# Optimization experiments

Hardware: AMD Instinct MI355X
Metric: run time of the kernel (lower is better)

The kernel has to match this reference:

```python
import jax, jax.numpy as jnp
import numpy as np

B, T, D, H = 1024, 365, 24, 128
OUT_DIMS = (1, 3, 3, 2)
GRU_IN = (D, D + 1, 2 * H, 2 * H)


def _uniform(k, shape, bound):
    return jax.random.uniform(k, shape, jnp.float32, -bound, bound)


def setup_inputs() -> dict:
    key = jax.random.key(0)
    inp = {"x": jax.random.normal(jax.random.fold_in(key, 0), (B, T, D), jnp.float32)}
    s = 1.0 / float(np.sqrt(H))  # torch GRUCell/Linear default init scale
    i = 1
    for c in range(4):
        inp[f"Wih{c+1}"] = _uniform(jax.random.fold_in(key, i), (3 * H, GRU_IN[c]), s); i += 1
        inp[f"Whh{c+1}"] = _uniform(jax.random.fold_in(key, i), (3 * H, H), s); i += 1
        inp[f"bih{c+1}"] = _uniform(jax.random.fold_in(key, i), (3 * H,), s); i += 1
        inp[f"bhh{c+1}"] = _uniform(jax.random.fold_in(key, i), (3 * H,), s); i += 1
        inp[f"Wfc{c+1}"] = _uniform(jax.random.fold_in(key, i), (OUT_DIMS[c], H), s); i += 1
        inp[f"bfc{c+1}"] = _uniform(jax.random.fold_in(key, i), (OUT_DIMS[c],), s); i += 1
    return inp


def _gru_cell(xt, h, Wih, Whh, bih, bhh):
    # PyTorch GRUCell: r,z,n gate order
    gi = xt @ Wih.T + bih
    gh = h @ Whh.T + bhh
    ir, iz, inn = jnp.split(gi, 3, axis=-1)
    hr, hz, hn = jnp.split(gh, 3, axis=-1)
    r = jax.nn.sigmoid(ir + hr)
    z = jax.nn.sigmoid(iz + hz)
    n = jnp.tanh(inn + r * hn)
    return (1.0 - z) * n + z * h


def _forward(x, Wih1, Whh1, bih1, bhh1, Wfc1, bfc1,
             Wih2, Whh2, bih2, bhh2, Wfc2, bfc2,
             Wih3, Whh3, bih3, bhh3, Wfc3, bfc3,
             Wih4, Whh4, bih4, bhh4, Wfc4, bfc4):
    b = x.shape[0]
    sg = jax.lax.stop_gradient
    h0 = jnp.zeros((b, H), x.dtype)
    lai0 = jnp.zeros((b, 1), x.dtype)  # LAI_previous starts at zero, always detached

    def step(carry, xt):
        h1, h2, h3, h4, lai = carry
        h1 = _gru_cell(xt, h1, Wih1, Whh1, bih1, bhh1)
        h2 = _gru_cell(jnp.concatenate([xt, lai], axis=1), h2, Wih2, Whh2, bih2, bhh2)
        o1 = h1 @ Wfc1.T + bfc1
        o2 = h2 @ Wfc2.T + bfc2
        h3 = _gru_cell(jnp.concatenate([sg(h1), sg(h2)], axis=1), h3, Wih3, Whh3, bih3, bhh3)
        o3 = h3 @ Wfc3.T + bfc3
        h4 = _gru_cell(jnp.concatenate([sg(h1), sg(h3)], axis=1), h4, Wih4, Whh4, bih4, bhh4)
        o4 = h4 @ Wfc4.T + bfc4
        lai = sg(o4[:, :1])
        return (h1, h2, h3, h4, lai), (jnp.concatenate([o1, o2, o3, o4], axis=1), h1, h2, h3, h4)

    (h1f, h2f, h3f, h4f, _), ys = jax.lax.scan(step, (h0, h0, h0, h0, lai0), jnp.swapaxes(x, 0, 1))
    out_t, hT1, hT2, hT3, hT4 = ys  # each [T, B, .]
    to_bt = lambda a: jnp.swapaxes(a, 0, 1)
    return (to_bt(out_t), h1f, h2f, h3f, h4f, to_bt(hT1), to_bt(hT2), to_bt(hT3), to_bt(hT4))


def reference(x, Wih1, Whh1, bih1, bhh1, Wfc1, bfc1,
              Wih2, Whh2, bih2, bhh2, Wfc2, bfc2,
              Wih3, Whh3, bih3, bhh3, Wfc3, bfc3,
              Wih4, Whh4, bih4, bhh4, Wfc4, bfc4):
    return _forward(x, Wih1, Whh1, bih1, bhh1, Wfc1, bfc1,
                    Wih2, Whh2, bih2, bhh2, Wfc2, bfc2,
                    Wih3, Whh3, bih3, bhh3, Wfc3, bfc3,
                    Wih4, Whh4, bih4, bhh4, Wfc4, bfc4)
```

## Files before the change

kernel.cpp:

```cpp
#include <hip/hip_runtime.h>
#include <hip/hip_bf16.h>

#define B_ 1024
#define T_ 365
#define D_ 24
#define H_ 128
#define NG 32
#define NS 8
#define GB 32

#define SLICE_EL 52224
#define ARENA_EL (8 * SLICE_EL)

typedef __attribute__((ext_vector_type(8))) short bf16x8;
typedef __attribute__((ext_vector_type(4))) float f32x4;

__device__ __align__(16) unsigned short g_arena[ARENA_EL];
__device__ __align__(16) unsigned g_mb[4][NG][2048];
__device__ unsigned g_flags[NG][4];
__device__ unsigned g_tick[8];

#define MFMA(a, b, c) __builtin_amdgcn_mfma_f32_16x16x32_bf16((a), (b), (c), 0, 0, 0)

__device__ __forceinline__ bf16x8 ldw(const unsigned short* p) {
  return *(const bf16x8*)p;
}
__device__ __forceinline__ unsigned short f2b(float f) {
  union { __hip_bfloat16 h; unsigned short u; } cv;
  cv.h = __float2bfloat16(f);
  return cv.u;
}
__device__ __forceinline__ float b2f(unsigned short u) {
  union { float f; unsigned int u32; } cv;
  cv.u32 = ((unsigned int)u) << 16;
  return cv.f;
}
__device__ __forceinline__ float sigmoidf_(float x) { return 1.f / (1.f + __expf(-x)); }
__device__ __forceinline__ float tanhf_(float x) {
  float e = __expf(2.f * x);
  return 1.f - 2.f / (e + 1.f);
}

__device__ __forceinline__ void st_l2(unsigned* p, unsigned v) {
  asm volatile("global_store_dword %0, %1, off sc0" :: "v"(p), "v"(v) : "memory");
}
__device__ __forceinline__ unsigned ld_dev(const unsigned* p) {
  unsigned v;
  asm volatile("global_load_dword %0, %1, off sc0 sc1\n\ts_waitcnt vmcnt(0)"
               : "=v"(v) : "v"(p) : "memory");
  return v;
}

__global__ void prep_weights(const float* wih1, const float* wih2,
                             const float* wih3, const float* wih4,
                             const float* whh1, const float* whh2,
                             const float* whh3, const float* whh4) {
  int i = blockIdx.x * blockDim.x + threadIdx.x;
  if (i < NG * 4) ((unsigned*)g_flags)[i] = 0;
  if (i < 8) g_tick[i] = 0;
  if (i >= ARENA_EL) return;
  int s = i / SLICE_EL, r = i % SLICE_EL;
  int tile = r >> 9, wi = r & 511;
  int khi = wi >> 7, nlo = (wi >> 3) & 15, e = wi & 7;
  float v = 0.f;
  if (tile < 3) {
    int row = tile * 128 + s * 16 + nlo, k = khi * 8 + e;
    if (k < 24) v = wih1[row * 24 + k];
  } else if (tile < 6) {
    int row = (tile - 3) * 128 + s * 16 + nlo, k = khi * 8 + e;
    if (k < 25) v = wih2[row * 25 + k];
  } else if (tile < 18) {
    int tt = tile - 6; int row = (tt >> 2) * 128 + s * 16 + nlo;
    v = whh1[row * 128 + (tt & 3) * 32 + khi * 8 + e];
  } else if (tile < 30) {
    int tt = tile - 18; int row = (tt >> 2) * 128 + s * 16 + nlo;
    v = whh2[row * 128 + (tt & 3) * 32 + khi * 8 + e];
  } else if (tile < 54) {
    int tt = tile - 30; int row = (tt >> 3) * 128 + s * 16 + nlo;
    v = wih3[row * 256 + (tt & 7) * 32 + khi * 8 + e];
  } else if (tile < 66) {
    int tt = tile - 54; int row = (tt >> 2) * 128 + s * 16 + nlo;
    v = whh3[row * 128 + (tt & 3) * 32 + khi * 8 + e];
  } else if (tile < 90) {
    int tt = tile - 66; int row = (tt >> 3) * 128 + s * 16 + nlo;
    v = wih4[row * 256 + (tt & 7) * 32 + khi * 8 + e];
  } else {
    int tt = tile - 90; int row = (tt >> 2) * 128 + s * 16 + nlo;
    v = whh4[row * 128 + (tt & 3) * 32 + khi * 8 + e];
  }
  g_arena[i] = f2b(v);
}

struct P {
  const float* x;
  const float* bih[4];
  const float* bhh[4];
  const float* wfc[4];
  const float* bfc[4];
  float* out;
  float* hf[4];
  float* hT[4];
};

__device__ __forceinline__ void gsync(int g, int st, unsigned target) {
  asm volatile("s_waitcnt vmcnt(0)" ::: "memory");
  __syncthreads();
  if (threadIdx.x == 0) {
    __hip_atomic_fetch_add(&g_flags[g][st], 1u, __ATOMIC_RELAXED, __HIP_MEMORY_SCOPE_AGENT);
    const unsigned* fp = &g_flags[g][st];
    unsigned v = ld_dev(fp);
    unsigned spins = 0;
    while (v < target && ++spins < (1u << 22)) {
      __builtin_amdgcn_s_sleep(2);
      v = ld_dev(fp);
    }
  }
  __syncthreads();
}

#define L_WSL  0u
#define L_HBUF 104448u
#define L_PSUM 137216u
#define L_XA   145408u
#define L_FCW  147456u
#define SMEMB  152064u

__global__ __launch_bounds__(256, 1) void gru_main(P p) {
  extern __shared__ __align__(16) unsigned char smem[];
  unsigned short* wsl = (unsigned short*)(smem + L_WSL);
  unsigned short* hbuf = (unsigned short*)(smem + L_HBUF);
  float* psum = (float*)(smem + L_PSUM);
  unsigned short* xa = (unsigned short*)(smem + L_XA);
  float (*fcw)[H_] = (float (*)[H_])(smem + L_FCW);

  const int tid = threadIdx.x;
  const int lane = tid & 63;
  const int w = tid >> 6;
  const int nlo = lane & 15, khi = lane >> 4;

  int* meta = (int*)psum;
  if (tid == 0) {
    unsigned xcc = __builtin_amdgcn_s_getreg((3 << 11) | 20) & 7;
    unsigned tk = __hip_atomic_fetch_add(&g_tick[xcc], 1u,
                                         __ATOMIC_RELAXED, __HIP_MEMORY_SCOPE_AGENT);
    tk &= 31;
    meta[0] = (int)(xcc * 4 + (tk >> 3));
    meta[1] = (int)(tk & 7);
  }
  __syncthreads();
  const int g = meta[0], s = meta[1];
  __syncthreads();

  const int b0 = g * GB;
  const int wkoff = khi * 128 + nlo * 8;
  const int hkoff = khi * 256 + nlo * 8;
  const int row = tid >> 3, cp = tid & 7;
  const int col0 = s * 16 + cp * 2;
  const int mbw = (col0 >> 3) * 128 + row * 4 + ((col0 & 7) >> 1);

  { const uint4* srcw = (const uint4*)(g_arena + s * SLICE_EL);
    uint4* dstw = (uint4*)wsl;
    for (int i = tid; i < SLICE_EL / 8; i += 256) dstw[i] = srcw[i]; }
  for (int i = tid; i < 8192; i += 256) ((unsigned*)hbuf)[i] = 0;
  for (int i = tid; i < 1024; i += 256) {
    int kg = i >> 8, rem = i & 255, r2 = rem >> 3, e = i & 7;
    int c = kg * 8 + e;
    unsigned short vv = 0;
    if (c < 24) vv = f2b(p.x[(size_t)(b0 + r2) * (T_ * D_) + c]);
    xa[i] = vv;
  }
  for (int i = tid; i < 9 * H_; i += 256) {
    int rw = i >> 7, k = i & 127;
    const float* srcf; int lr;
    if (rw == 0)      { srcf = p.wfc[0]; lr = 0; }
    else if (rw < 4)  { srcf = p.wfc[1]; lr = rw - 1; }
    else if (rw < 7)  { srcf = p.wfc[2]; lr = rw - 4; }
    else              { srcf = p.wfc[3]; lr = rw - 7; }
    fcw[rw][k] = srcf[lr * H_ + k];
  }

  float bR[4][2], bZ[4][2], bI[4][2], bHn[4][2], hreg[4][2];
#pragma unroll
  for (int c = 0; c < 4; ++c)
#pragma unroll
    for (int j = 0; j < 2; ++j) {
      int cc = col0 + j;
      bR[c][j]  = p.bih[c][cc] + p.bhh[c][cc];
      bZ[c][j]  = p.bih[c][H_ + cc] + p.bhh[c][H_ + cc];
      bI[c][j]  = p.bih[c][2 * H_ + cc];
      bHn[c][j] = p.bhh[c][2 * H_ + cc];
      hreg[c][j] = 0.f;
    }
  const float bfc7 = p.bfc[3][0];
  const float bfc8 = p.bfc[3][1];
  int fc_c = 0; float fcb = 0.f;
  if (s == 0)      { fc_c = 0; fcb = p.bfc[0][0]; }
  else if (s < 4)  { fc_c = 1; fcb = p.bfc[1][s - 1]; }
  else if (s < 7)  { fc_c = 2; fcb = p.bfc[2][s - 4]; }

  float* hTp[4];
#pragma unroll
  for (int c = 0; c < 4; ++c)
    hTp[c] = p.hT[c] + (size_t)(b0 + row) * (T_ * H_) + col0;
  float* outp = p.out + (size_t)(b0 + row) * (T_ * 9);

  const f32x4 zf = {0.f, 0.f, 0.f, 0.f};

#define WF(tt)        ldw(wsl + (tt) * 512 + wkoff)
#define HF(c, kc, mt) ldw(hbuf + (c) * 4096 + (kc) * 1024 + (mt) * 128 + hkoff)
#define XF(mt)        ldw(xa + (mt) * 128 + hkoff)
#define PWR(slot, mt, v) do { \
  float* pp_ = psum + (slot) * 512 + (mt) * 256 + khi * 64 + nlo; \
  pp_[0] = (v)[0]; pp_[16] = (v)[1]; pp_[32] = (v)[2]; pp_[48] = (v)[3]; \
} while (0)

#define STAGE_A(C, TWX, THX) do { \
  if (w < 2) { \
    _Pragma("unroll") \
    for (int mt = 0; mt < 2; ++mt) { \
      f32x4 acc = MFMA(XF(mt), WF((TWX) + w), zf); \
      _Pragma("unroll") \
      for (int kc = 0; kc < 4; ++kc) acc = MFMA(HF(C, kc, mt), WF((THX) + w * 4 + kc), acc); \
      PWR(w, mt, acc); \
    } \
  } else if (w == 2) { \
    _Pragma("unroll") \
    for (int mt = 0; mt < 2; ++mt) { f32x4 acc = MFMA(XF(mt), WF((TWX) + 2), zf); PWR(2, mt, acc); } \
  } else { \
    _Pragma("unroll") \
    for (int mt = 0; mt < 2; ++mt) { \
      f32x4 acc = zf; \
      _Pragma("unroll") \
      for (int kc = 0; kc < 4; ++kc) acc = MFMA(HF(C, kc, mt), WF((THX) + 8 + kc), acc); \
      PWR(3, mt, acc); \
    } \
  } \
} while (0)

#define STAGE_BC(CA, CB, CH, TWX, THX) do { \
  if (w < 2) { \
    _Pragma("unroll") \
    for (int mt = 0; mt < 2; ++mt) { \
      f32x4 acc = zf; \
      _Pragma("unroll") \
      for (int kc = 0; kc < 4; ++kc) acc = MFMA(HF(CA, kc, mt), WF((TWX) + w * 8 + kc), acc); \
      _Pragma("unroll") \
      for (int kc = 0; kc < 4; ++kc) acc = MFMA(HF(CB, kc, mt), WF((TWX) + w * 8 + 4 + kc), acc); \
      _Pragma("unroll") \
      for (int kc = 0; kc < 4; ++kc) acc = MFMA(HF(CH, kc, mt), WF((THX) + w * 4 + kc), acc); \
      PWR(w, mt, acc); \
    } \
  } else if (w == 2) { \
    _Pragma("unroll") \
    for (int mt = 0; mt < 2; ++mt) { \
      f32x4 acc = zf; \
      _Pragma("unroll") \
      for (int kc = 0; kc < 4; ++kc) acc = MFMA(HF(CA, kc, mt), WF((TWX) + 16 + kc), acc); \
      _Pragma("unroll") \
      for (int kc = 0; kc < 4; ++kc) acc = MFMA(HF(CB, kc, mt), WF((TWX) + 16 + 4 + kc), acc); \
      PWR(2, mt, acc); \
    } \
  } else { \
    _Pragma("unroll") \
    for (int mt = 0; mt < 2; ++mt) { \
      f32x4 acc = zf; \
      _Pragma("unroll") \
      for (int kc = 0; kc < 4; ++kc) acc = MFMA(HF(CH, kc, mt), WF((THX) + 8 + kc), acc); \
      PWR(3, mt, acc); \
    } \
  } \
} while (0)

#define FIN(C) do { \
  const float* pb_ = psum + (row >> 4) * 256 + (row & 15) * 16 + cp * 2; \
  float R0 = pb_[0],    Ra = pb_[1]; \
  float Z0 = pb_[512],  Za = pb_[513]; \
  float I0 = pb_[1024], Ia = pb_[1025]; \
  float G0 = pb_[1536], Ga = pb_[1537]; \
  float r0 = sigmoidf_(R0 + bR[C][0]), r1 = sigmoidf_(Ra + bR[C][1]); \
  float z0 = sigmoidf_(Z0 + bZ[C][0]), z1 = sigmoidf_(Za + bZ[C][1]); \
  float n0 = tanhf_(I0 + bI[C][0] + r0 * (G0 + bHn[C][0])); \
  float n1 = tanhf_(Ia + bI[C][1] + r1 * (Ga + bHn[C][1])); \
  float h0 = (1.f - z0) * n0 + z0 * hreg[C][0]; \
  float h1 = (1.f - z1) * n1 + z1 * hreg[C][1]; \
  hreg[C][0] = h0; hreg[C][1] = h1; \
  unsigned pk_ = (unsigned)f2b(h0) | ((unsigned)f2b(h1) << 16); \
  st_l2(&g_mb[C][g][0] + mbw, pk_); \
  union { float f[2]; unsigned long long u; } cv_; \
  cv_.f[0] = h0; cv_.f[1] = h1; \
  __builtin_nontemporal_store(cv_.u, (unsigned long long*)hTp[C]); \
  hTp[C] += H_; \
} while (0)

#define COPYMB(C) do { \
  const uint4* sm_ = (const uint4*)&g_mb[C][g][0]; \
  uint4 va_, vb_; \
  asm volatile("global_load_dwordx4 %0, %2, off sc0\n\t" \
               "global_load_dwordx4 %1, %3, off sc0\n\t" \
               "s_waitcnt vmcnt(0)" \
               : "=&v"(va_), "=&v"(vb_) \
               : "v"(sm_ + tid), "v"(sm_ + tid + 256) : "memory"); \
  uint4* dm_ = (uint4*)(hbuf + (C) * 4096); \
  dm_[tid] = va_; dm_[tid + 256] = vb_; \
} while (0)

  __syncthreads();

  for (int t = 0; t < T_; ++t) {
    STAGE_A(0, 0, 6);
    __syncthreads();
    FIN(0);
    __syncthreads();
    STAGE_A(1, 3, 18);
    __syncthreads();
    FIN(1);
    gsync(g, 0, 8u * (t + 1));

    COPYMB(0); COPYMB(1);
    __syncthreads();
    STAGE_BC(0, 1, 2, 30, 54);
    __syncthreads();
    FIN(2);
    gsync(g, 1, 8u * (t + 1));

    COPYMB(2);
    __syncthreads();
    STAGE_BC(0, 2, 3, 66, 90);
    __syncthreads();
    FIN(3);
    gsync(g, 2, 8u * (t + 1));

    COPYMB(3);
    if (t + 1 < T_) {
      for (int i = tid; i < GB * D_; i += 256) {
        int r2 = i / D_, cc = i % D_;
        xa[(cc >> 3) * 256 + r2 * 8 + (cc & 7)] =
            f2b(p.x[(size_t)(b0 + r2) * (T_ * D_) + (size_t)(t + 1) * D_ + cc]);
      }
    }
    __syncthreads();
    {
      float hx[16];
      const unsigned short* hp = hbuf + 3 * 4096 + (cp * 2) * 256 + row * 8;
      bf16x8 v0 = ldw(hp), v1 = ldw(hp + 256);
#pragma unroll
      for (int e = 0; e < 8; ++e) {
        hx[e] = b2f((unsigned short)v0[e]);
        hx[8 + e] = b2f((unsigned short)v1[e]);
      }
      float acc = 0.f;
#pragma unroll
      for (int j = 0; j < 16; ++j) acc += hx[j] * fcw[7][cp * 16 + j];
      acc += __shfl_xor(acc, 1); acc += __shfl_xor(acc, 2); acc += __shfl_xor(acc, 4);
      float laiv = acc + bfc7;
      if (cp == 0) {
        xa[3 * 256 + row * 8] = f2b(laiv);
        if (s == 7) __builtin_nontemporal_store(laiv, outp + (size_t)t * 9 + 7);
      }
      if (s == 0) {
        float a8 = 0.f;
#pragma unroll
        for (int j = 0; j < 16; ++j) a8 += hx[j] * fcw[8][cp * 16 + j];
        a8 += __shfl_xor(a8, 1); a8 += __shfl_xor(a8, 2); a8 += __shfl_xor(a8, 4);
        if (cp == 0) __builtin_nontemporal_store(a8 + bfc8, outp + (size_t)t * 9 + 8);
      }
      if (s < 7) {
        const unsigned short* hq = hbuf + fc_c * 4096 + (cp * 2) * 256 + row * 8;
        bf16x8 u0 = ldw(hq), u1 = ldw(hq + 256);
        float a = 0.f;
#pragma unroll
        for (int j = 0; j < 8; ++j) a += b2f((unsigned short)u0[j]) * fcw[s][cp * 16 + j];
#pragma unroll
        for (int j = 0; j < 8; ++j) a += b2f((unsigned short)u1[j]) * fcw[s][cp * 16 + 8 + j];
        a += __shfl_xor(a, 1); a += __shfl_xor(a, 2); a += __shfl_xor(a, 4);
        if (cp == 0) __builtin_nontemporal_store(a + fcb, outp + (size_t)t * 9 + s);
      }
    }
    __syncthreads();
  }

#pragma unroll
  for (int c = 0; c < 4; ++c) {
    union { float f[2]; unsigned long long u; } cv;
    cv.f[0] = hreg[c][0]; cv.f[1] = hreg[c][1];
    __builtin_nontemporal_store(cv.u,
        (unsigned long long*)(p.hf[c] + (size_t)(b0 + row) * H_ + col0));
  }
}

extern "C" void kernel_launch(void* const* d_in, const int* in_sizes, int n_in,
                              void* d_out, int out_size, void* d_ws, size_t ws_size,
                              hipStream_t stream) {
  (void)in_sizes; (void)n_in; (void)d_ws; (void)ws_size; (void)out_size;
  const float* x    = (const float*)d_in[0];
  const float* wih1 = (const float*)d_in[1];
  const float* whh1 = (const float*)d_in[2];
  const float* wih2 = (const float*)d_in[7];
  const float* whh2 = (const float*)d_in[8];
  const float* wih3 = (const float*)d_in[13];
  const float* whh3 = (const float*)d_in[14];
  const float* wih4 = (const float*)d_in[19];
  const float* whh4 = (const float*)d_in[20];

  prep_weights<<<(ARENA_EL + 255) / 256, 256, 0, stream>>>(
      wih1, wih2, wih3, wih4, whh1, whh2, whh3, whh4);

  P p;
  p.x = x;
  for (int c = 0; c < 4; ++c) {
    p.bih[c] = (const float*)d_in[3 + 6 * c];
    p.bhh[c] = (const float*)d_in[4 + 6 * c];
    p.wfc[c] = (const float*)d_in[5 + 6 * c];
    p.bfc[c] = (const float*)d_in[6 + 6 * c];
  }
  float* out = (float*)d_out;
  p.out = out;
  const size_t HF_OFF = (size_t)B_ * T_ * 9;
  const size_t HT_OFF = HF_OFF + 4ull * B_ * H_;
  const size_t HT_SZ  = (size_t)B_ * T_ * H_;
  for (int c = 0; c < 4; ++c) {
    p.hf[c] = out + HF_OFF + (size_t)c * B_ * H_;
    p.hT[c] = out + HT_OFF + (size_t)c * HT_SZ;
  }

  (void)hipFuncSetAttribute(reinterpret_cast<const void*>(gru_main),
                            hipFuncAttributeMaxDynamicSharedMemorySize, (int)SMEMB);
  gru_main<<<NG * NS, 256, SMEMB, stream>>>(p);
}
```

Before: 4.357 ms.

## Use LDS-only barriers, defer hT stores, and remove sleep in grid spin-wait

Replaces __syncthreads with a custom barrier that waits only on LDS counters (lgkmcnt) rather than vector memory, so outstanding global stores no longer stall each intra-step barrier. The per-step hT stores move out of FIN into one batch after the last stage, and output stores use inline-asm nontemporal stores so the compiler cannot insert vmcnt waits. The s_sleep in the inter-block spin loop is removed to cut wake-up latency, at the cost of more polling traffic on the flag.

```diff
diff --git a/kernel.cpp b/kernel.cpp
--- a/kernel.cpp
+++ b/kernel.cpp
@@ -21,6 +21,13 @@
 __device__ unsigned g_tick[8];
 
 #define MFMA(a, b, c) __builtin_amdgcn_mfma_f32_16x16x32_bf16((a), (b), (c), 0, 0, 0)
+
+#define BAR() do { \
+  __builtin_amdgcn_sched_barrier(0); \
+  asm volatile("s_waitcnt lgkmcnt(0)" ::: "memory"); \
+  __builtin_amdgcn_s_barrier(); \
+  __builtin_amdgcn_sched_barrier(0); \
+} while (0)
 
 __device__ __forceinline__ bf16x8 ldw(const unsigned short* p) {
   return *(const bf16x8*)p;
@@ -111,7 +118,6 @@
     unsigned v = ld_dev(fp);
     unsigned spins = 0;
     while (v < target && ++spins < (1u << 22)) {
-      __builtin_amdgcn_s_sleep(2);
       v = ld_dev(fp);
     }
   }
@@ -286,10 +292,6 @@
   hreg[C][0] = h0; hreg[C][1] = h1; \
   unsigned pk_ = (unsigned)f2b(h0) | ((unsigned)f2b(h1) << 16); \
   st_l2(&g_mb[C][g][0] + mbw, pk_); \
-  union { float f[2]; unsigned long long u; } cv_; \
-  cv_.f[0] = h0; cv_.f[1] = h1; \
-  __builtin_nontemporal_store(cv_.u, (unsigned long long*)hTp[C]); \
-  hTp[C] += H_; \
 } while (0)
 
 #define COPYMB(C) do { \
@@ -308,25 +310,25 @@
 
   for (int t = 0; t < T_; ++t) {
     STAGE_A(0, 0, 6);
-    __syncthreads();
+    BAR();
     FIN(0);
-    __syncthreads();
+    BAR();
     STAGE_A(1, 3, 18);
-    __syncthreads();
+    BAR();
     FIN(1);
     gsync(g, 0, 8u * (t + 1));
 
     COPYMB(0); COPYMB(1);
-    __syncthreads();
+    BAR();
     STAGE_BC(0, 1, 2, 30, 54);
-    __syncthreads();
+    BAR();
     FIN(2);
     gsync(g, 1, 8u * (t + 1));
 
     COPYMB(2);
-    __syncthreads();
+    BAR();
     STAGE_BC(0, 2, 3, 66, 90);
-    __syncthreads();
+    BAR();
     FIN(3);
     gsync(g, 2, 8u * (t + 1));
 
@@ -338,7 +340,15 @@
             f2b(p.x[(size_t)(b0 + r2) * (T_ * D_) + (size_t)(t + 1) * D_ + cc]);
       }
     }
-    __syncthreads();
+#pragma unroll
+    for (int c = 0; c < 4; ++c) {
+      union { float f[2]; unsigned long long u; } cv;
+      cv.f[0] = hreg[c][0]; cv.f[1] = hreg[c][1];
+      asm volatile("global_store_dwordx2 %0, %1, off nt"
+                   :: "v"(hTp[c]), "v"(cv.u) : "memory");
+      hTp[c] += H_;
+    }
+    BAR();
     {
       float hx[16];
       const unsigned short* hp = hbuf + 3 * 4096 + (cp * 2) * 256 + row * 8;
@@ -355,14 +365,21 @@
       float laiv = acc + bfc7;
       if (cp == 0) {
         xa[3 * 256 + row * 8] = f2b(laiv);
-        if (s == 7) __builtin_nontemporal_store(laiv, outp + (size_t)t * 9 + 7);
+        if (s == 7) {
+          float* op_ = outp + (size_t)t * 9 + 7;
+          asm volatile("global_store_dword %0, %1, off nt" :: "v"(op_), "v"(laiv) : "memory");
+        }
       }
       if (s == 0) {
         float a8 = 0.f;
 #pragma unroll
         for (int j = 0; j < 16; ++j) a8 += hx[j] * fcw[8][cp * 16 + j];
         a8 += __shfl_xor(a8, 1); a8 += __shfl_xor(a8, 2); a8 += __shfl_xor(a8, 4);
-        if (cp == 0) __builtin_nontemporal_store(a8 + bfc8, outp + (size_t)t * 9 + 8);
+        if (cp == 0) {
+          float v8 = a8 + bfc8;
+          float* op_ = outp + (size_t)t * 9 + 8;
+          asm volatile("global_store_dword %0, %1, off nt" :: "v"(op_), "v"(v8) : "memory");
+        }
       }
       if (s < 7) {
         const unsigned short* hq = hbuf + fc_c * 4096 + (cp * 2) * 256 + row * 8;
@@ -373,19 +390,24 @@
 #pragma unroll
         for (int j = 0; j < 8; ++j) a += b2f((unsigned short)u1[j]) * fcw[s][cp * 16 + 8 + j];
         a += __shfl_xor(a, 1); a += __shfl_xor(a, 2); a += __shfl_xor(a, 4);
-        if (cp == 0) __builtin_nontemporal_store(a + fcb, outp + (size_t)t * 9 + s);
+        if (cp == 0) {
+          float vs = a + fcb;
+          float* op_ = outp + (size_t)t * 9 + s;
+          asm volatile("global_store_dword %0, %1, off nt" :: "v"(op_), "v"(vs) : "memory");
+        }
       }
     }
-    __syncthreads();
+    BAR();
   }
 
 #pragma unroll
   for (int c = 0; c < 4; ++c) {
     union { float f[2]; unsigned long long u; } cv;
     cv.f[0] = hreg[c][0]; cv.f[1] = hreg[c][1];
-    __builtin_nontemporal_store(cv.u,
-        (unsigned long long*)(p.hf[c] + (size_t)(b0 + row) * H_ + col0));
-  }
+    asm volatile("global_store_dwordx2 %0, %1, off nt"
+                 :: "v"(p.hf[c] + (size_t)(b0 + row) * H_ + col0), "v"(cv.u) : "memory");
+  }
+  asm volatile("s_waitcnt vmcnt(0)" ::: "memory");
 }
 
 extern "C" void kernel_launch(void* const* d_in, const int* in_sizes, int n_in,
```

Result: faster. 4.189 ms (-3.8%).
